# Kernel tuning notes

Hardware: AMD Instinct MI355X
Metric: run time of the kernel (lower is better)

The kernel has to match this reference:

```python
import jax, jax.numpy as jnp
import numpy as np

# Balanced binary-tree tensorized circuit (CP sum-product layers), cirkit-style.
B, D, C, K, NCLS = 256, 256, 1, 256, 10
LEVELS = 8  # log2(D); each level halves the number of regions


def setup_inputs() -> dict:
    key = jax.random.key(0)
    ks = jax.random.split(key, LEVELS + 3)
    inp = {"x": jax.random.normal(ks[0], (B, D, C), dtype=jnp.float32)}
    # Input layer params: per-variable linear map C -> K units
    inp["W_in"] = jax.random.normal(ks[1], (D, C, K), dtype=jnp.float32)
    # CP layer params per tree level: (n_regions, arity=2, K_in, K_out)
    n = D
    for l in range(LEVELS):
        n //= 2
        inp[f"W_lvl{l}"] = jax.random.normal(ks[2 + l], (n, 2, K, K), dtype=jnp.float32)
    # Output mixing layer K -> num_classes
    inp["W_out"] = jax.random.normal(ks[2 + LEVELS], (K, NCLS), dtype=jnp.float32)
    return inp


def _circuit(x, W_in, W_lvls, W_out):
    # Input layers: gather scope (here: each var is its own scope) + per-var map.
    # (B, D, C) x (D, C, K) -> (B, D, K); tanh keeps units bounded in [-1, 1].
    h = jnp.tanh(jnp.einsum('bdc,dck->bdk', x, W_in))
    # Fused sum-product (CP) layers, one batched einsum per tree level instead of
    # a Python loop over individual small layers.
    for W in W_lvls:
        n = W.shape[0]
        hp = h.reshape(h.shape[0], n, 2, K)          # pair adjacent regions
        Wn = jax.nn.softmax(W, axis=2)               # reparam: convex sum over K_in
        proj = jnp.einsum('bnak,nakj->bnaj', hp, Wn) # per-child sum layer
        h = proj[:, :, 0, :] * proj[:, :, 1, :]      # Hadamard product layer
    root = h[:, 0, :]                                # (B, K)
    out = jnp.einsum('bk,kc->bc', root, jax.nn.softmax(W_out, axis=0))
    return out[:, None, :]                           # (B, num_out=1, num_cls)


def reference(x, W_in, W_lvl0, W_lvl1, W_lvl2, W_lvl3, W_lvl4, W_lvl5, W_lvl6, W_lvl7, W_out):
    W_lvls = [W_lvl0, W_lvl1, W_lvl2, W_lvl3, W_lvl4, W_lvl5, W_lvl6, W_lvl7]
    return _circuit(x, W_in, W_lvls, W_out)
```

## Files before the change

### kernel.cpp

```cpp
#include <hip/hip_runtime.h>
#include <stdint.h>

#define Kk 256
#define NCLS 10

typedef __attribute__((ext_vector_type(8))) short short8;
typedef __attribute__((ext_vector_type(4))) float f32x4;

__device__ __forceinline__ float bf2f(ushort u) {
    return __uint_as_float(((unsigned int)u) << 16);
}
__device__ __forceinline__ ushort f2bf(float f) {
    unsigned int u = __float_as_uint(f);
    u = (u + 0x7FFFu + ((u >> 16) & 1u)) >> 16;
    return (ushort)u;
}
__device__ __forceinline__ float tanh_fast(float v) {
    float t = __expf(2.f * v);
    return (t - 1.f) / (t + 1.f);
}
__device__ __forceinline__ void gll16(const void* g, void* s) {
    __builtin_amdgcn_global_load_lds(
        (const __attribute__((address_space(1))) void*)g,
        (__attribute__((address_space(3))) void*)s, 16, 0, 0);
}

__device__ void exp_tile(const float* __restrict__ Wb, ushort* __restrict__ Eb,
                         float* __restrict__ rcp_row, const int j0)
{
    __shared__ float sT[64][68];
    __shared__ float sC[4][64];
    const int tid = threadIdx.x;
    const int lj = tid & 63;
    const int kq = tid >> 6;
    const int jj = (tid & 15) * 4;
    const int kk = tid >> 4;
    float csum = 0.f;

    for (int kb = 0; kb < 4; ++kb) {
        #pragma unroll
        for (int p = 0; p < 4; ++p) {
            const int k = kb * 64 + p * 16 + kk;
            *(float4*)&sT[p * 16 + kk][jj] = *(const float4*)&Wb[(size_t)k * 256 + j0 + jj];
        }
        __syncthreads();
        ushort pk[16];
        #pragma unroll
        for (int t = 0; t < 16; ++t) {
            const float e = __expf(sT[kq * 16 + t][lj]);
            csum += e;
            pk[t] = f2bf(e);
        }
        short8 v0, v1;
        #pragma unroll
        for (int e2 = 0; e2 < 8; ++e2) { v0[e2] = (short)pk[e2]; v1[e2] = (short)pk[8 + e2]; }
        ushort* dst = Eb + (size_t)(j0 + lj) * 256 + kb * 64 + kq * 16;
        *(short8*)dst = v0;
        *(short8*)(dst + 8) = v1;
        __syncthreads();
    }
    sC[kq][lj] = csum;
    __syncthreads();
    if (tid < 64)
        rcp_row[j0 + tid] = 1.f / (sC[0][tid] + sC[1][tid] + sC[2][tid] + sC[3][tid]);
}

__global__ __launch_bounds__(256)
void exp0_kernel(const float* __restrict__ W, ushort* __restrict__ E,
                 float* __restrict__ Rcp)
{
    const int ia = blockIdx.y;
    const int j0 = blockIdx.x * 64;
    exp_tile(W + (size_t)ia * 65536, E + ((size_t)ia << 16),
             Rcp + (size_t)ia * 256, j0);
}

__global__ __launch_bounds__(256)
void exp_rest_kernel(const float* __restrict__ W1, const float* __restrict__ W2,
                     const float* __restrict__ W3, const float* __restrict__ W4,
                     const float* __restrict__ W5, const float* __restrict__ W6,
                     const float* __restrict__ W7,
                     ushort* __restrict__ Ebase, float* __restrict__ RcpBase)
{
    int rem = blockIdx.x;
    int lvl = 1, n2 = 128;
    while (rem >= n2 * 4 && lvl < 7) { rem -= n2 * 4; n2 >>= 1; ++lvl; }
    const int jt = rem & 3;
    const int ia = rem >> 2;
    const float* W;
    switch (lvl) {
        case 1: W = W1; break; case 2: W = W2; break; case 3: W = W3; break;
        case 4: W = W4; break; case 5: W = W5; break; case 6: W = W6; break;
        default: W = W7; break;
    }
    size_t eoff = 0; int rrow = 256;
    for (int m = 1; m < lvl; ++m) { eoff += ((size_t)(256 >> m)) << 16; rrow += (256 >> m); }
    exp_tile(W + (size_t)ia * 65536,
             Ebase + eoff + ((size_t)ia << 16),
             RcpBase + (size_t)(rrow + ia) * 256, jt * 64);
}

template<bool TANH>
__global__ __launch_bounds__(256, 3)
void level_kernel(const float* __restrict__ x,
                  const float* __restrict__ Win,
                  const ushort* __restrict__ H,
                  const ushort* __restrict__ E,
                  const float* __restrict__ Rcp,
                  ushort* __restrict__ Hout,
                  const int n)
{
    __shared__ __align__(16) char sA[2][2][128 * 64];
    __shared__ __align__(16) char sE[2][2][64 * 64];

    const int tid = threadIdx.x;
    const int bh  = blockIdx.x & 1;
    const int jt  = blockIdx.x >> 1;
    const int i   = blockIdx.y;
    const int b0  = bh * 128;
    const int j0  = jt * 64;
    const int np  = 2 * n;

    const int l   = tid & 63;
    const int l15 = l & 15;
    const int g   = l >> 4;
    const int w   = tid >> 6;
    const int wm  = w >> 1;
    const int wn  = w & 1;

    f32x4 acc[2][4][2];
    #pragma unroll
    for (int a2 = 0; a2 < 2; ++a2)
        #pragma unroll
        for (int mf = 0; mf < 4; ++mf)
            #pragma unroll
            for (int nf = 0; nf < 2; ++nf)
                acc[a2][mf][nf] = (f32x4){0.f, 0.f, 0.f, 0.f};

    float xv = 0.f;
    const int ta   = tid >> 7;
    const int trow = tid & 127;
    if (TANH) xv = x[(size_t)(b0 + trow) * 256 + (2 * i + ta)];

    auto stage = [&](int buf, int k0) {
        if (TANH) {
            const float* wrow = &Win[(size_t)(2 * i + ta) * 256 + k0];
            char* base = &sA[ta][buf][trow * 64];
            const int sr = (trow >> 1) & 3;
            #pragma unroll
            for (int c = 0; c < 4; ++c) {
                const float4 w0 = *(const float4*)&wrow[c * 8];
                const float4 w1 = *(const float4*)&wrow[c * 8 + 4];
                short8 v;
                v[0] = (short)f2bf(tanh_fast(xv * w0.x));
                v[1] = (short)f2bf(tanh_fast(xv * w0.y));
                v[2] = (short)f2bf(tanh_fast(xv * w0.z));
                v[3] = (short)f2bf(tanh_fast(xv * w0.w));
                v[4] = (short)f2bf(tanh_fast(xv * w1.x));
                v[5] = (short)f2bf(tanh_fast(xv * w1.y));
                v[6] = (short)f2bf(tanh_fast(xv * w1.z));
                v[7] = (short)f2bf(tanh_fast(xv * w1.w));
                *(short8*)(base + (((c ^ sr)) << 4)) = v;
            }
        } else {
            #pragma unroll
            for (int u0 = 0; u0 < 4; ++u0) {
                const int u   = w * 4 + u0;
                const int ua  = u >> 3;
                const int r16 = (u & 7) << 4;
                const int row = r16 + (l >> 2);
                const int c   = l & 3;
                const ushort* src = H
                    + ((size_t)(b0 + row) * np + (2 * i + ua)) * 256
                    + k0 + ((c ^ ((row >> 1) & 3)) << 3);
                gll16(src, &sA[ua][buf][r16 * 64]);
            }
        }
        #pragma unroll
        for (int v0 = 0; v0 < 2; ++v0) {
            const int v    = w * 2 + v0;
            const int ea   = v >> 2;
            const int jr16 = (v & 3) << 4;
            const int jr   = jr16 + (l >> 2);
            const int c    = l & 3;
            const ushort* src = E + ((size_t)(2 * i + ea) << 16)
                + (size_t)(j0 + jr) * 256
                + k0 + ((c ^ ((jr >> 1) & 3)) << 3);
            gll16(src, &sE[ea][buf][jr16 * 64]);
        }
    };

    stage(0, 0);
    __syncthreads();

    for (int t = 0; t < 8; ++t) {
        const int buf = t & 1;
        if (t < 7) stage(buf ^ 1, (t + 1) * 32);

        short8 afr[2][4];
        short8 bfr[2][2];
        #pragma unroll
        for (int a2 = 0; a2 < 2; ++a2) {
            #pragma unroll
            for (int nf = 0; nf < 2; ++nf) {
                const int jr = wn * 32 + nf * 16 + l15;
                bfr[a2][nf] = *(const short8*)&sE[a2][buf][jr * 64 + ((g ^ ((jr >> 1) & 3)) << 4)];
            }
            #pragma unroll
            for (int mf = 0; mf < 4; ++mf) {
                const int row = wm * 64 + mf * 16 + l15;
                afr[a2][mf] = *(const short8*)&sA[a2][buf][row * 64 + ((g ^ ((row >> 1) & 3)) << 4)];
            }
        }
        #pragma unroll
        for (int a2 = 0; a2 < 2; ++a2)
            #pragma unroll
            for (int mf = 0; mf < 4; ++mf)
                #pragma unroll
                for (int nf = 0; nf < 2; ++nf)
                    acc[a2][mf][nf] = __builtin_amdgcn_mfma_f32_16x16x32_bf16(
                        afr[a2][mf], bfr[a2][nf], acc[a2][mf][nf], 0, 0, 0);
        __syncthreads();
    }

    float rc[2][2];
    #pragma unroll
    for (int a2 = 0; a2 < 2; ++a2)
        #pragma unroll
        for (int nf = 0; nf < 2; ++nf)
            rc[a2][nf] = Rcp[(size_t)(2 * i + a2) * 256 + j0 + wn * 32 + nf * 16 + l15];

    #pragma unroll
    for (int mf = 0; mf < 4; ++mf)
        #pragma unroll
        for (int nf = 0; nf < 2; ++nf) {
            const int j = j0 + wn * 32 + nf * 16 + l15;
            #pragma unroll
            for (int r = 0; r < 4; ++r) {
                const int b = b0 + wm * 64 + mf * 16 + g * 4 + r;
                const float v0 = acc[0][mf][nf][r] * rc[0][nf];
                const float v1 = acc[1][mf][nf][r] * rc[1][nf];
                Hout[((size_t)b * n + i) * 256 + j] = f2bf(v0 * v1);
            }
        }
}

__global__ __launch_bounds__(256)
void out_kernel(const ushort* __restrict__ root, const float* __restrict__ Wout,
                float* __restrict__ out)
{
    __shared__ float sR[16][260];
    __shared__ float sE2[256][12];
    __shared__ float sDen[16];
    const int tid = threadIdx.x;
    if (tid < 16) sDen[tid] = 0.f;
    __syncthreads();
    float e[NCLS];
    #pragma unroll
    for (int c = 0; c < NCLS; ++c) {
        e[c] = __expf(Wout[(size_t)tid * NCLS + c]);
        sE2[tid][c] = e[c];
    }
    #pragma unroll
    for (int c = 0; c < NCLS; ++c) {
        float v = e[c];
        for (int off = 32; off > 0; off >>= 1) v += __shfl_down(v, off);
        if ((tid & 63) == 0) atomicAdd(&sDen[c], v);
    }
    const int b0 = blockIdx.x * 16;
    #pragma unroll
    for (int v = 0; v < 4; ++v) {
        const int u = v * 256 + tid;
        const int row = u >> 6;
        const int c4 = (u & 63) * 4;
        const ushort4 p = *(const ushort4*)&root[(size_t)(b0 + row) * 256 + c4];
        sR[row][c4 + 0] = bf2f(p.x);
        sR[row][c4 + 1] = bf2f(p.y);
        sR[row][c4 + 2] = bf2f(p.z);
        sR[row][c4 + 3] = bf2f(p.w);
    }
    __syncthreads();
    const int ty = tid >> 4, tx = tid & 15;
    if (tx < NCLS) {
        float s = 0.f;
        for (int k = 0; k < Kk; ++k) s += sR[ty][k] * sE2[k][tx];
        out[(size_t)(b0 + ty) * NCLS + tx] = s / sDen[tx];
    }
}

extern "C" void kernel_launch(void* const* d_in, const int* in_sizes, int n_in,
                              void* d_out, int out_size, void* d_ws, size_t ws_size,
                              hipStream_t stream)
{
    const float* x    = (const float*)d_in[0];
    const float* Win  = (const float*)d_in[1];
    const float* Wl[8];
    for (int lv = 0; lv < 8; ++lv) Wl[lv] = (const float*)d_in[2 + lv];
    const float* Wout = (const float*)d_in[10];
    float* out = (float*)d_out;

    char* wsb = (char*)d_ws;
    ushort* R1 = (ushort*)wsb;
    ushort* R2 = (ushort*)(wsb + 33554432);
    ushort* R3 = (ushort*)(wsb + 50331648);
    float*  RC = (float*)(wsb + 58720256);

    exp0_kernel<<<dim3(4, 256), 256, 0, stream>>>(Wl[0], R1, RC);
    level_kernel<true><<<dim3(8, 128), 256, 0, stream>>>(x, Win, nullptr, R1, RC, R2, 128);
    exp_rest_kernel<<<dim3(1016), 256, 0, stream>>>(Wl[1], Wl[2], Wl[3], Wl[4],
                                                    Wl[5], Wl[6], Wl[7], R1, RC);
    size_t eoff = 0;
    size_t rrow = 256;
    const ushort* hin = R2;
    ushort* hout = nullptr;
    for (int lv = 1; lv < 8; ++lv) {
        const int n = 128 >> lv;
        hout = (lv & 1) ? R3 : R2;
        level_kernel<false><<<dim3(8, n), 256, 0, stream>>>(
            nullptr, nullptr, hin, R1 + eoff, RC + rrow * 256, hout, n);
        hin = hout;
        eoff += ((size_t)(2 * n)) << 16;
        rrow += 2 * n;
    }
    out_kernel<<<dim3(16), 256, 0, stream>>>(hin, Wout, out);
}
```

Before: 313.8 us.

## Precompute tanh input layer in prep kernel and shrink batch tiles at deep levels

```diff
diff --git a/kernel.cpp b/kernel.cpp
--- a/kernel.cpp
+++ b/kernel.cpp
@@ -1,7 +1,5 @@
 #include <hip/hip_runtime.h>
-#include <stdint.h>
-
-#define Kk 256
+
 #define NCLS 10
 
 typedef __attribute__((ext_vector_type(8))) short short8;
@@ -66,6 +64,35 @@
 }
 
 __global__ __launch_bounds__(256)
+void prep1_kernel(const float* __restrict__ W0, const float* __restrict__ x,
+                  const float* __restrict__ Win, ushort* __restrict__ E0,
+                  float* __restrict__ Rcp0, ushort* __restrict__ H0)
+{
+    const int bid = blockIdx.x;
+    if (bid < 1024) {
+        const int ia = bid >> 2, jt = bid & 3;
+        exp_tile(W0 + (size_t)ia * 65536, E0 + ((size_t)ia << 16),
+                 Rcp0 + (size_t)ia * 256, jt * 64);
+    } else {
+        __shared__ float sX[256];
+        const int d = bid - 1024;
+        const int tid = threadIdx.x;
+        sX[tid] = x[(size_t)tid * 256 + d];
+        __syncthreads();
+        const int k2 = (tid & 127) * 2;
+        const int boff = tid >> 7;
+        const float2 wv = *(const float2*)&Win[(size_t)d * 256 + k2];
+        for (int b2 = 0; b2 < 256; b2 += 2) {
+            const int b = b2 + boff;
+            const float xb = sX[b];
+            const unsigned int u0 = f2bf(tanh_fast(xb * wv.x));
+            const unsigned int u1 = f2bf(tanh_fast(xb * wv.y));
+            *(unsigned int*)&H0[((size_t)b * 256 + d) * 256 + k2] = u0 | (u1 << 16);
+        }
+    }
+}
+
+__global__ __launch_bounds__(256)
 void exp0_kernel(const float* __restrict__ W, ushort* __restrict__ E,
                  float* __restrict__ Rcp)
 {
@@ -76,11 +103,11 @@
 }
 
 __global__ __launch_bounds__(256)
-void exp_rest_kernel(const float* __restrict__ W1, const float* __restrict__ W2,
-                     const float* __restrict__ W3, const float* __restrict__ W4,
-                     const float* __restrict__ W5, const float* __restrict__ W6,
-                     const float* __restrict__ W7,
-                     ushort* __restrict__ Ebase, float* __restrict__ RcpBase)
+void prep2_kernel(const float* __restrict__ W1, const float* __restrict__ W2,
+                  const float* __restrict__ W3, const float* __restrict__ W4,
+                  const float* __restrict__ W5, const float* __restrict__ W6,
+                  const float* __restrict__ W7,
+                  ushort* __restrict__ Ebase, float* __restrict__ RcpBase)
 {
     int rem = blockIdx.x;
     int lvl = 1, n2 = 128;
@@ -100,24 +127,27 @@
              RcpBase + (size_t)(rrow + ia) * 256, jt * 64);
 }
 
-template<bool TANH>
-__global__ __launch_bounds__(256, 3)
-void level_kernel(const float* __restrict__ x,
-                  const float* __restrict__ Win,
-                  const ushort* __restrict__ H,
-                  const ushort* __restrict__ E,
-                  const float* __restrict__ Rcp,
-                  ushort* __restrict__ Hout,
+template<int BM, int WR, int WC, int LB, bool TANH>
+__global__ __launch_bounds__(256, LB)
+void level_kernel(const float* __restrict__ x, const float* __restrict__ Win,
+                  const ushort* __restrict__ H, const ushort* __restrict__ E,
+                  const float* __restrict__ Rcp, ushort* __restrict__ Hout,
                   const int n)
 {
-    __shared__ __align__(16) char sA[2][2][128 * 64];
-    __shared__ __align__(16) char sE[2][2][64 * 64];
+    constexpr int MF = BM / (16 * WR);
+    constexpr int NF = 64 / (16 * WC);
+    constexpr int NBH = 256 / BM;
+    constexpr int AUNITS = 2 * BM / 16;
+    constexpr int UITER = (AUNITS + 3) / 4;
+
+    __shared__ __align__(16) char sA[2][2][BM * 64];
+    __shared__ __align__(16) char sB[2][2][64 * 64];
 
     const int tid = threadIdx.x;
-    const int bh  = blockIdx.x & 1;
-    const int jt  = blockIdx.x >> 1;
+    const int bh  = blockIdx.x % NBH;
+    const int jt  = blockIdx.x / NBH;
     const int i   = blockIdx.y;
-    const int b0  = bh * 128;
+    const int b0  = bh * BM;
     const int j0  = jt * 64;
     const int np  = 2 * n;
 
@@ -125,25 +155,27 @@
     const int l15 = l & 15;
     const int g   = l >> 4;
     const int w   = tid >> 6;
-    const int wm  = w >> 1;
-    const int wn  = w & 1;
-
-    f32x4 acc[2][4][2];
+    const int wm  = w / WC;
+    const int wn  = w % WC;
+
+    f32x4 acc[2][MF][NF];
     #pragma unroll
     for (int a2 = 0; a2 < 2; ++a2)
         #pragma unroll
-        for (int mf = 0; mf < 4; ++mf)
-            #pragma unroll
-            for (int nf = 0; nf < 2; ++nf)
+        for (int mf = 0; mf < MF; ++mf)
+            #pragma unroll
+            for (int nf = 0; nf < NF; ++nf)
                 acc[a2][mf][nf] = (f32x4){0.f, 0.f, 0.f, 0.f};
 
     float xv = 0.f;
-    const int ta   = tid >> 7;
-    const int trow = tid & 127;
-    if (TANH) xv = x[(size_t)(b0 + trow) * 256 + (2 * i + ta)];
+    int ta = 0, trow = 0;
+    if (TANH) {
+        ta = tid >> 7; trow = tid & 127;
+        xv = x[(size_t)(b0 + trow) * 256 + 2 * i + ta];
+    }
 
     auto stage = [&](int buf, int k0) {
-        if (TANH) {
+        if constexpr (TANH) {
             const float* wrow = &Win[(size_t)(2 * i + ta) * 256 + k0];
             char* base = &sA[ta][buf][trow * 64];
             const int sr = (trow >> 1) & 3;
@@ -160,33 +192,35 @@
                 v[5] = (short)f2bf(tanh_fast(xv * w1.y));
                 v[6] = (short)f2bf(tanh_fast(xv * w1.z));
                 v[7] = (short)f2bf(tanh_fast(xv * w1.w));
-                *(short8*)(base + (((c ^ sr)) << 4)) = v;
+                *(short8*)(base + ((c ^ sr) << 4)) = v;
             }
         } else {
             #pragma unroll
-            for (int u0 = 0; u0 < 4; ++u0) {
-                const int u   = w * 4 + u0;
-                const int ua  = u >> 3;
-                const int r16 = (u & 7) << 4;
-                const int row = r16 + (l >> 2);
-                const int c   = l & 3;
-                const ushort* src = H
-                    + ((size_t)(b0 + row) * np + (2 * i + ua)) * 256
-                    + k0 + ((c ^ ((row >> 1) & 3)) << 3);
-                gll16(src, &sA[ua][buf][r16 * 64]);
-            }
-        }
-        #pragma unroll
-        for (int v0 = 0; v0 < 2; ++v0) {
-            const int v    = w * 2 + v0;
+            for (int uu = 0; uu < UITER; ++uu) {
+                const int u = w + uu * 4;
+                if (u < AUNITS) {
+                    const int ua  = u / (BM / 16);
+                    const int r16 = (u % (BM / 16)) * 16;
+                    const int row = r16 + (l >> 2);
+                    const int c   = l & 3;
+                    const ushort* src = H
+                        + ((size_t)(b0 + row) * np + (2 * i + ua)) * 256
+                        + k0 + ((c ^ ((row >> 1) & 3)) << 3);
+                    gll16(src, &sA[ua][buf][r16 * 64]);
+                }
+            }
+        }
+        #pragma unroll
+        for (int vv = 0; vv < 2; ++vv) {
+            const int v    = w + vv * 4;
             const int ea   = v >> 2;
-            const int jr16 = (v & 3) << 4;
+            const int jr16 = (v & 3) * 16;
             const int jr   = jr16 + (l >> 2);
             const int c    = l & 3;
             const ushort* src = E + ((size_t)(2 * i + ea) << 16)
                 + (size_t)(j0 + jr) * 256
                 + k0 + ((c ^ ((jr >> 1) & 3)) << 3);
-            gll16(src, &sE[ea][buf][jr16 * 64]);
+            gll16(src, &sB[ea][buf][jr16 * 64]);
         }
     };
 
@@ -197,47 +231,47 @@
         const int buf = t & 1;
         if (t < 7) stage(buf ^ 1, (t + 1) * 32);
 
-        short8 afr[2][4];
-        short8 bfr[2][2];
+        short8 afr[2][MF];
+        short8 bfr[2][NF];
         #pragma unroll
         for (int a2 = 0; a2 < 2; ++a2) {
             #pragma unroll
-            for (int nf = 0; nf < 2; ++nf) {
-                const int jr = wn * 32 + nf * 16 + l15;
-                bfr[a2][nf] = *(const short8*)&sE[a2][buf][jr * 64 + ((g ^ ((jr >> 1) & 3)) << 4)];
-            }
-            #pragma unroll
-            for (int mf = 0; mf < 4; ++mf) {
-                const int row = wm * 64 + mf * 16 + l15;
+            for (int nf = 0; nf < NF; ++nf) {
+                const int jr = wn * (NF * 16) + nf * 16 + l15;
+                bfr[a2][nf] = *(const short8*)&sB[a2][buf][jr * 64 + ((g ^ ((jr >> 1) & 3)) << 4)];
+            }
+            #pragma unroll
+            for (int mf = 0; mf < MF; ++mf) {
+                const int row = wm * (MF * 16) + mf * 16 + l15;
                 afr[a2][mf] = *(const short8*)&sA[a2][buf][row * 64 + ((g ^ ((row >> 1) & 3)) << 4)];
             }
         }
         #pragma unroll
         for (int a2 = 0; a2 < 2; ++a2)
             #pragma unroll
-            for (int mf = 0; mf < 4; ++mf)
+            for (int mf = 0; mf < MF; ++mf)
                 #pragma unroll
-                for (int nf = 0; nf < 2; ++nf)
+                for (int nf = 0; nf < NF; ++nf)
                     acc[a2][mf][nf] = __builtin_amdgcn_mfma_f32_16x16x32_bf16(
                         afr[a2][mf], bfr[a2][nf], acc[a2][mf][nf], 0, 0, 0);
         __syncthreads();
     }
 
-    float rc[2][2];
+    float rc[2][NF];
     #pragma unroll
     for (int a2 = 0; a2 < 2; ++a2)
         #pragma unroll
-        for (int nf = 0; nf < 2; ++nf)
-            rc[a2][nf] = Rcp[(size_t)(2 * i + a2) * 256 + j0 + wn * 32 + nf * 16 + l15];
-
-    #pragma unroll
-    for (int mf = 0; mf < 4; ++mf)
-        #pragma unroll
-        for (int nf = 0; nf < 2; ++nf) {
-            const int j = j0 + wn * 32 + nf * 16 + l15;
+        for (int nf = 0; nf < NF; ++nf)
+            rc[a2][nf] = Rcp[(size_t)(2 * i + a2) * 256 + j0 + wn * (NF * 16) + nf * 16 + l15];
+
+    #pragma unroll
+    for (int mf = 0; mf < MF; ++mf)
+        #pragma unroll
+        for (int nf = 0; nf < NF; ++nf) {
+            const int j = j0 + wn * (NF * 16) + nf * 16 + l15;
             #pragma unroll
             for (int r = 0; r < 4; ++r) {
-                const int b = b0 + wm * 64 + mf * 16 + g * 4 + r;
+                const int b = b0 + wm * (MF * 16) + mf * 16 + g * 4 + r;
                 const float v0 = acc[0][mf][nf][r] * rc[0][nf];
                 const float v1 = acc[1][mf][nf][r] * rc[1][nf];
                 Hout[((size_t)b * n + i) * 256 + j] = f2bf(v0 * v1);
@@ -283,7 +317,7 @@
     const int ty = tid >> 4, tx = tid & 15;
     if (tx < NCLS) {
         float s = 0.f;
-        for (int k = 0; k < Kk; ++k) s += sR[ty][k] * sE2[k][tx];
+        for (int k = 0; k < 256; ++k) s += sR[ty][k] * sE2[k][tx];
         out[(size_t)(b0 + ty) * NCLS + tx] = s / sDen[tx];
     }
 }
@@ -300,27 +334,62 @@
     float* out = (float*)d_out;
 
     char* wsb = (char*)d_ws;
-    ushort* R1 = (ushort*)wsb;
-    ushort* R2 = (ushort*)(wsb + 33554432);
-    ushort* R3 = (ushort*)(wsb + 50331648);
-    float*  RC = (float*)(wsb + 58720256);
-
-    exp0_kernel<<<dim3(4, 256), 256, 0, stream>>>(Wl[0], R1, RC);
-    level_kernel<true><<<dim3(8, 128), 256, 0, stream>>>(x, Win, nullptr, R1, RC, R2, 128);
-    exp_rest_kernel<<<dim3(1016), 256, 0, stream>>>(Wl[1], Wl[2], Wl[3], Wl[4],
-                                                    Wl[5], Wl[6], Wl[7], R1, RC);
-    size_t eoff = 0;
-    size_t rrow = 256;
-    const ushort* hin = R2;
-    ushort* hout = nullptr;
-    for (int lv = 1; lv < 8; ++lv) {
-        const int n = 128 >> lv;
-        hout = (lv & 1) ? R3 : R2;
-        level_kernel<false><<<dim3(8, n), 256, 0, stream>>>(
-            nullptr, nullptr, hin, R1 + eoff, RC + rrow * 256, hout, n);
-        hin = hout;
-        eoff += ((size_t)(2 * n)) << 16;
-        rrow += 2 * n;
-    }
-    out_kernel<<<dim3(16), 256, 0, stream>>>(hin, Wout, out);
-}
+    static const size_t ecum[8] = {0, 0, 128, 192, 224, 240, 248, 252};
+
+    if (ws_size >= 84408320ull) {
+        ushort* A0 = (ushort*)wsb;
+        ushort* A1 = (ushort*)(wsb + 16777216);
+        ushort* C  = (ushort*)(wsb + 33554432);
+        ushort* B  = (ushort*)(wsb + 50331648);
+        float*  RC = (float*)(wsb + 83886080);
+
+        prep1_kernel<<<dim3(1280), 256, 0, stream>>>(Wl[0], x, Win, A0, RC, B);
+        level_kernel<128, 2, 2, 3, false><<<dim3(8, 128), 256, 0, stream>>>(
+            nullptr, nullptr, B, A0, RC, C, 128);
+        prep2_kernel<<<dim3(1016), 256, 0, stream>>>(
+            Wl[1], Wl[2], Wl[3], Wl[4], Wl[5], Wl[6], Wl[7], B, RC);
+
+        level_kernel<64, 2, 2, 4, false><<<dim3(16, 64), 256, 0, stream>>>(
+            nullptr, nullptr, C, B + (ecum[1] << 16), RC + (256 + ecum[1]) * 256, A0, 64);
+        level_kernel<64, 2, 2, 4, false><<<dim3(16, 32), 256, 0, stream>>>(
+            nullptr, nullptr, A0, B + (ecum[2] << 16), RC + (256 + ecum[2]) * 256, A1, 32);
+        level_kernel<32, 2, 2, 4, false><<<dim3(32, 16), 256, 0, stream>>>(
+            nullptr, nullptr, A1, B + (ecum[3] << 16), RC + (256 + ecum[3]) * 256, A0, 16);
+        level_kernel<32, 2, 2, 4, false><<<dim3(32, 8), 256, 0, stream>>>(
+            nullptr, nullptr, A0, B + (ecum[4] << 16), RC + (256 + ecum[4]) * 256, A1, 8);
+        level_kernel<16, 1, 4, 4, false><<<dim3(64, 4), 256, 0, stream>>>(
+            nullptr, nullptr, A1, B + (ecum[5] << 16), RC + (256 + ecum[5]) * 256, A0, 4);
+        level_kernel<16, 1, 4, 4, false><<<dim3(64, 2), 256, 0, stream>>>(
+            nullptr, nullptr, A0, B + (ecum[6] << 16), RC + (256 + ecum[6]) * 256, A1, 2);
+        level_kernel<16, 1, 4, 4, false><<<dim3(64, 1), 256, 0, stream>>>(
+            nullptr, nullptr, A1, B + (ecum[7] << 16), RC + (256 + ecum[7]) * 256, A0, 1);
+        out_kernel<<<dim3(16), 256, 0, stream>>>(A0, Wout, out);
+    } else {
+        ushort* R1 = (ushort*)wsb;
+        ushort* R2 = (ushort*)(wsb + 33554432);
+        ushort* R3 = (ushort*)(wsb + 50331648);
+        float*  RC = (float*)(wsb + 58720256);
+
+        exp0_kernel<<<dim3(4, 256), 256, 0, stream>>>(Wl[0], R1, RC);
+        level_kernel<128, 2, 2, 3, true><<<dim3(8, 128), 256, 0, stream>>>(
+            x, Win, nullptr, R1, RC, R2, 128);
+        prep2_kernel<<<dim3(1016), 256, 0, stream>>>(
+            Wl[1], Wl[2], Wl[3], Wl[4], Wl[5], Wl[6], Wl[7], R1, RC);
+
+        level_kernel<64, 2, 2, 4, false><<<dim3(16, 64), 256, 0, stream>>>(
+            nullptr, nullptr, R2, R1 + (ecum[1] << 16), RC + (256 + ecum[1]) * 256, R3, 64);
+        level_kernel<64, 2, 2, 4, false><<<dim3(16, 32), 256, 0, stream>>>(
+            nullptr, nullptr, R3, R1 + (ecum[2] << 16), RC + (256 + ecum[2]) * 256, R2, 32);
+        level_kernel<32, 2, 2, 4, false><<<dim3(32, 16), 256, 0, stream>>>(
+            nullptr, nullptr, R2, R1 + (ecum[3] << 16), RC + (256 + ecum[3]) * 256, R3, 16);
+        level_kernel<32, 2, 2, 4, false><<<dim3(32, 8), 256, 0, stream>>>(
+            nullptr, nullptr, R3, R1 + (ecum[4] << 16), RC + (256 + ecum[4]) * 256, R2, 8);
+        level_kernel<16, 1, 4, 4, false><<<dim3(64, 4), 256, 0, stream>>>(
+            nullptr, nullptr, R2, R1 + (ecum[5] << 16), RC + (256 + ecum[5]) * 256, R3, 4);
+        level_kernel<16, 1, 4, 4, false><<<dim3(64, 2), 256, 0, stream>>>(
+            nullptr, nullptr, R3, R1 + (ecum[6] << 16), RC + (256 + ecum[6]) * 256, R2, 2);
+        level_kernel<16, 1, 4, 4, false><<<dim3(64, 1), 256, 0, stream>>>(
+            nullptr, nullptr, R2, R1 + (ecum[7] << 16), RC + (256 + ecum[7]) * 256, R3, 1);
+        out_kernel<<<dim3(16), 256, 0, stream>>>(R3, Wout, out);
+    }
+}
```

Result: faster. 307.3 us (-2.1%).
